# Performance work log

Hardware: AMD Instinct MI355X
Metric: run time of the kernel (lower is better)

## Reference

```python
import jax, jax.numpy as jnp
import numpy as np

B, T, H, LD = 32, 2048, 1024, 1024

def setup_inputs() -> dict:
    key = jax.random.key(0)
    k1, k2, k3, k4, k5 = jax.random.split(key, 5)
    scale = 1.0 / np.sqrt(H)
    return {
        "encoder_hidden": jax.random.normal(k1, (B, T, H), dtype=jnp.float32),
        "decoder_hidden": jax.random.normal(k2, (B, H), dtype=jnp.float32),
        "W1": jax.random.normal(k3, (H, LD), dtype=jnp.float32) * scale,
        "b1": jnp.zeros((LD,), dtype=jnp.float32),
        "W2": jax.random.normal(k4, (H, LD), dtype=jnp.float32) * scale,
        "b2": jnp.zeros((LD,), dtype=jnp.float32),
        "V": jax.random.normal(k5, (LD, 1), dtype=jnp.float32) * (1.0 / np.sqrt(LD)),
        "bV": jnp.zeros((1,), dtype=jnp.float32),
    }

def reference(encoder_hidden, decoder_hidden, W1, b1, W2, b2, V, bV):
    # dec proj: [B, 1, ld]
    dec_w = (decoder_hidden @ W1 + b1)[:, None, :]
    # enc proj: [B, T, ld]
    enc_w = jnp.einsum('bth,hl->btl', encoder_hidden, W2) + b2
    # multiplicative combine (as in source: decoder_Weight * encoder_weight)
    score = jnp.tanh(dec_w * enc_w) @ V + bV          # [B, T, 1]
    attn = jax.nn.softmax(score, axis=1)              # softmax over time
    context = jnp.sum(attn * encoder_hidden, axis=1)  # [B, H]
    return context, attn
```

## Files before the change

kernel.cpp:

```cpp
#include <hip/hip_runtime.h>
#include <hip/hip_bf16.h>
#include <math.h>

#define B_  32
#define T_  2048
#define H_  1024
#define LD_ 1024
#define M_  (B_*T_)

typedef __attribute__((ext_vector_type(8))) short bf16x8;
typedef __attribute__((ext_vector_type(4))) float f32x4;

__device__ __forceinline__ void async_copy16(void* lds, const void* g) {
  __builtin_amdgcn_global_load_lds(
      (const __attribute__((address_space(1))) void*)g,
      (__attribute__((address_space(3))) void*)lds, 16, 0, 0);
}

__global__ void convert_w2(const float* __restrict__ W2, __hip_bfloat16* __restrict__ w2p) {
  int idx = blockIdx.x * 256 + threadIdx.x;
  int kg = idx >> 10, n = idx & 1023;
  __align__(16) __hip_bfloat16 h[8];
#pragma unroll
  for (int j = 0; j < 8; ++j)
    h[j] = __float2bfloat16(W2[(size_t)(kg * 8 + j) * LD_ + n]);
  *reinterpret_cast<uint4*>(&w2p[(size_t)kg * (LD_ * 8) + n * 8]) =
      *reinterpret_cast<const uint4*>(h);
}

__global__ void dec_proj(const float* __restrict__ dec, const float* __restrict__ W1,
                         const float* __restrict__ b1, float* __restrict__ dec_w) {
  __shared__ float sdec[H_];
  int bb = blockIdx.x >> 2;
  int l = (blockIdx.x & 3) * 256 + threadIdx.x;
  for (int i = threadIdx.x; i < H_; i += 256) sdec[i] = dec[bb * H_ + i];
  __syncthreads();
  float a0 = 0.f, a1 = 0.f, a2 = 0.f, a3 = 0.f;
  for (int h = 0; h < H_; h += 4) {
    a0 += sdec[h + 0] * W1[(h + 0) * LD_ + l];
    a1 += sdec[h + 1] * W1[(h + 1) * LD_ + l];
    a2 += sdec[h + 2] * W1[(h + 2) * LD_ + l];
    a3 += sdec[h + 3] * W1[(h + 3) * LD_ + l];
  }
  dec_w[bb * LD_ + l] = (a0 + a1) + (a2 + a3) + b1[l];
}

__global__ __launch_bounds__(256, 2)
void score_gemm(const float* __restrict__ enc,
                const __hip_bfloat16* __restrict__ w2p,
                const float* __restrict__ dec_w,
                const float* __restrict__ b2,
                const float* __restrict__ V,
                float* __restrict__ score) {
  __shared__ __align__(16) __hip_bfloat16 Asm[4][128][8];
  __shared__ __align__(16) __hip_bfloat16 Bsm[4][256][8];

  const int tid  = threadIdx.x;
  const int lane = tid & 63;
  const int wave = tid >> 6;
  const int wm = wave >> 1, wn = wave & 1;
  const int nb = blockIdx.x, mb = blockIdx.y;
  const int row0 = mb * 128, col0 = nb * 256;
  const int q = lane >> 4, c15 = lane & 15;

  f32x4 acc[4][8] = {};

  const int sm  = tid >> 2;
  const int skg = tid & 3;

  for (int k0 = 0; k0 < H_; k0 += 32) {
#pragma unroll
    for (int pass = 0; pass < 2; ++pass) {
      int m = pass * 64 + sm;
      const float4* src = reinterpret_cast<const float4*>(
          enc + (size_t)(row0 + m) * H_ + k0 + skg * 8);
      float4 f0 = src[0], f1 = src[1];
      __align__(16) __hip_bfloat16 h[8];
      h[0] = __float2bfloat16(f0.x); h[1] = __float2bfloat16(f0.y);
      h[2] = __float2bfloat16(f0.z); h[3] = __float2bfloat16(f0.w);
      h[4] = __float2bfloat16(f1.x); h[5] = __float2bfloat16(f1.y);
      h[6] = __float2bfloat16(f1.z); h[7] = __float2bfloat16(f1.w);
      *reinterpret_cast<uint4*>(&Asm[skg][m][0]) = *reinterpret_cast<const uint4*>(h);
    }
    {
      char* bbase = (char*)&Bsm[0][0][0];
      const char* gbase = (const char*)w2p + ((size_t)(k0 >> 3)) * (LD_ * 8 * 2)
                          + (size_t)col0 * 16 + tid * 16;
#pragma unroll
      for (int p = 0; p < 4; ++p)
        async_copy16(bbase + p * 4096 + tid * 16, gbase + (size_t)p * (LD_ * 8 * 2));
    }
    __syncthreads();

    bf16x8 af[4], bfr[8];
#pragma unroll
    for (int i = 0; i < 4; ++i)
      af[i] = *reinterpret_cast<const bf16x8*>(&Asm[q][wm * 64 + i * 16 + c15][0]);
#pragma unroll
    for (int j = 0; j < 8; ++j)
      bfr[j] = *reinterpret_cast<const bf16x8*>(&Bsm[q][wn * 128 + j * 16 + c15][0]);
#pragma unroll
    for (int i = 0; i < 4; ++i)
#pragma unroll
      for (int j = 0; j < 8; ++j)
        acc[i][j] = __builtin_amdgcn_mfma_f32_16x16x32_bf16(af[i], bfr[j], acc[i][j], 0, 0, 0);
    __syncthreads();
  }

  const int bb = row0 >> 11;
  float b2v[8], dwv[8], Vv[8];
#pragma unroll
  for (int j = 0; j < 8; ++j) {
    int n = col0 + wn * 128 + j * 16 + c15;
    b2v[j] = b2[n];
    dwv[j] = dec_w[bb * LD_ + n];
    Vv[j]  = V[n];
  }
#pragma unroll
  for (int i = 0; i < 4; ++i) {
#pragma unroll
    for (int r = 0; r < 4; ++r) {
      float v = 0.f;
#pragma unroll
      for (int j = 0; j < 8; ++j) {
        float e = acc[i][j][r] + b2v[j];
        v += tanhf(dwv[j] * e) * Vv[j];
      }
      v += __shfl_xor(v, 1);
      v += __shfl_xor(v, 2);
      v += __shfl_xor(v, 4);
      v += __shfl_xor(v, 8);
      if (c15 == 0) {
        int row = row0 + wm * 64 + i * 16 + q * 4 + r;
        atomicAdd(&score[row], v);
      }
    }
  }
}

__global__ void softmax_k(const float* __restrict__ score, float* __restrict__ attn) {
  int bb = blockIdx.x;
  int tid = threadIdx.x;
  int lane = tid & 63, wave = tid >> 6;
  __shared__ float red[4];
  float v[8];
  float mx = -3.4e38f;
#pragma unroll
  for (int i = 0; i < 8; ++i) {
    v[i] = score[bb * T_ + i * 256 + tid];
    mx = fmaxf(mx, v[i]);
  }
#pragma unroll
  for (int m = 32; m >= 1; m >>= 1) mx = fmaxf(mx, __shfl_xor(mx, m));
  if (lane == 0) red[wave] = mx;
  __syncthreads();
  mx = fmaxf(fmaxf(red[0], red[1]), fmaxf(red[2], red[3]));
  __syncthreads();
  float s = 0.f;
#pragma unroll
  for (int i = 0; i < 8; ++i) { v[i] = __expf(v[i] - mx); s += v[i]; }
#pragma unroll
  for (int m = 32; m >= 1; m >>= 1) s += __shfl_xor(s, m);
  if (lane == 0) red[wave] = s;
  __syncthreads();
  s = red[0] + red[1] + red[2] + red[3];
  float inv = 1.f / s;
#pragma unroll
  for (int i = 0; i < 8; ++i) attn[bb * T_ + i * 256 + tid] = v[i] * inv;
}

__global__ void context_k(const float* __restrict__ enc, const float* __restrict__ attn,
                          float* __restrict__ ctx) {
  int bb = blockIdx.y;
  int hc = blockIdx.x & 3, tc = blockIdx.x >> 2;
  int h = hc * 256 + threadIdx.x;
  __shared__ float sat[512];
  int t0 = tc * 512;
  for (int i = threadIdx.x; i < 512; i += 256) sat[i] = attn[bb * T_ + t0 + i];
  __syncthreads();
  const float* base = enc + ((size_t)bb * T_ + t0) * H_ + h;
  float a0 = 0.f, a1 = 0.f, a2 = 0.f, a3 = 0.f;
  for (int t = 0; t < 512; t += 4) {
    a0 += sat[t + 0] * base[(size_t)(t + 0) * H_];
    a1 += sat[t + 1] * base[(size_t)(t + 1) * H_];
    a2 += sat[t + 2] * base[(size_t)(t + 2) * H_];
    a3 += sat[t + 3] * base[(size_t)(t + 3) * H_];
  }
  atomicAdd(&ctx[bb * H_ + h], (a0 + a1) + (a2 + a3));
}

extern "C" void kernel_launch(void* const* d_in, const int* in_sizes, int n_in,
                              void* d_out, int out_size, void* d_ws, size_t ws_size,
                              hipStream_t stream) {
  const float* enc = (const float*)d_in[0];
  const float* dec = (const float*)d_in[1];
  const float* W1  = (const float*)d_in[2];
  const float* b1  = (const float*)d_in[3];
  const float* W2  = (const float*)d_in[4];
  const float* b2  = (const float*)d_in[5];
  const float* V   = (const float*)d_in[6];

  char* ws = (char*)d_ws;
  __hip_bfloat16* w2p = (__hip_bfloat16*)ws;
  float* dec_w = (float*)(ws + (2u << 20));
  float* score = (float*)(ws + (2u << 20) + (128u << 10));

  float* out  = (float*)d_out;
  float* ctx  = out;
  float* attn = out + B_ * H_;

  hipMemsetAsync(score, 0, (size_t)M_ * sizeof(float), stream);
  hipMemsetAsync(ctx, 0, (size_t)B_ * H_ * sizeof(float), stream);

  convert_w2<<<(H_ * LD_ / 8) / 256, 256, 0, stream>>>(W2, w2p);
  dec_proj<<<B_ * 4, 256, 0, stream>>>(dec, W1, b1, dec_w);
  score_gemm<<<dim3(LD_ / 256, M_ / 128), 256, 0, stream>>>(enc, w2p, dec_w, b2, V, score);
  softmax_k<<<B_, 256, 0, stream>>>(score, attn);
  context_k<<<dim3(16, B_), 256, 0, stream>>>(enc, attn, ctx);
}
```

Measured before the change: 641.0 us.

## Double-buffer score GEMM tiles, swizzle LDS and block order, vectorize context

The score GEMM now double-buffers its LDS tiles. The next fp32 encoder tile is prefetched into registers and the next W2 tile is fetched asynchronously while MFMAs run on the current buffer, leaving one barrier per k-step. The A tile's LDS row index is XOR-swizzled to cut bank conflicts, and the block index is remapped so that co-resident blocks share encoder rows in cache. The context kernel is rewritten to read float4 per thread over 128 time steps with wider accumulators, which costs more LDS and registers in the GEMM and may lower occupancy.

```diff
diff --git a/kernel.cpp b/kernel.cpp
--- a/kernel.cpp
+++ b/kernel.cpp
@@ -52,14 +52,16 @@
                 const float* __restrict__ b2,
                 const float* __restrict__ V,
                 float* __restrict__ score) {
-  __shared__ __align__(16) __hip_bfloat16 Asm[4][128][8];
-  __shared__ __align__(16) __hip_bfloat16 Bsm[4][256][8];
+  __shared__ __align__(16) __hip_bfloat16 Asm[2][4][128][8];
+  __shared__ __align__(16) __hip_bfloat16 Bsm[2][4][256][8];
 
   const int tid  = threadIdx.x;
   const int lane = tid & 63;
   const int wave = tid >> 6;
   const int wm = wave >> 1, wn = wave & 1;
-  const int nb = blockIdx.x, mb = blockIdx.y;
+  const int bid = blockIdx.y * gridDim.x + blockIdx.x;
+  const int swz = (bid & 7) * 256 + (bid >> 3);
+  const int mb = swz >> 2, nb = swz & 3;
   const int row0 = mb * 128, col0 = nb * 256;
   const int q = lane >> 4, c15 = lane & 15;
 
@@ -67,43 +69,69 @@
 
   const int sm  = tid >> 2;
   const int skg = tid & 3;
-
-  for (int k0 = 0; k0 < H_; k0 += 32) {
-#pragma unroll
-    for (int pass = 0; pass < 2; ++pass) {
-      int m = pass * 64 + sm;
-      const float4* src = reinterpret_cast<const float4*>(
-          enc + (size_t)(row0 + m) * H_ + k0 + skg * 8);
-      float4 f0 = src[0], f1 = src[1];
-      __align__(16) __hip_bfloat16 h[8];
-      h[0] = __float2bfloat16(f0.x); h[1] = __float2bfloat16(f0.y);
-      h[2] = __float2bfloat16(f0.z); h[3] = __float2bfloat16(f0.w);
-      h[4] = __float2bfloat16(f1.x); h[5] = __float2bfloat16(f1.y);
-      h[6] = __float2bfloat16(f1.z); h[7] = __float2bfloat16(f1.w);
-      *reinterpret_cast<uint4*>(&Asm[skg][m][0]) = *reinterpret_cast<const uint4*>(h);
+  const int sx  = skg * 2;
+
+  const size_t arow0 = (size_t)(row0 + sm) * H_ + skg * 8;
+  const size_t arow1 = (size_t)(row0 + 64 + sm) * H_ + skg * 8;
+
+  float4 pf[4];
+
+  auto LOADA = [&](int k0) {
+    pf[0] = *reinterpret_cast<const float4*>(enc + arow0 + k0);
+    pf[1] = *reinterpret_cast<const float4*>(enc + arow0 + k0 + 4);
+    pf[2] = *reinterpret_cast<const float4*>(enc + arow1 + k0);
+    pf[3] = *reinterpret_cast<const float4*>(enc + arow1 + k0 + 4);
+  };
+  auto CVTW = [&](int buf) {
+    __align__(16) __hip_bfloat16 h[8];
+    h[0] = __float2bfloat16(pf[0].x); h[1] = __float2bfloat16(pf[0].y);
+    h[2] = __float2bfloat16(pf[0].z); h[3] = __float2bfloat16(pf[0].w);
+    h[4] = __float2bfloat16(pf[1].x); h[5] = __float2bfloat16(pf[1].y);
+    h[6] = __float2bfloat16(pf[1].z); h[7] = __float2bfloat16(pf[1].w);
+    *reinterpret_cast<uint4*>(&Asm[buf][skg][sm ^ sx][0]) =
+        *reinterpret_cast<const uint4*>(h);
+    h[0] = __float2bfloat16(pf[2].x); h[1] = __float2bfloat16(pf[2].y);
+    h[2] = __float2bfloat16(pf[2].z); h[3] = __float2bfloat16(pf[2].w);
+    h[4] = __float2bfloat16(pf[3].x); h[5] = __float2bfloat16(pf[3].y);
+    h[6] = __float2bfloat16(pf[3].z); h[7] = __float2bfloat16(pf[3].w);
+    *reinterpret_cast<uint4*>(&Asm[buf][skg][(64 + sm) ^ sx][0]) =
+        *reinterpret_cast<const uint4*>(h);
+  };
+  auto GLOADB = [&](int buf, int k0) {
+    char* bbase = (char*)&Bsm[buf][0][0][0] + tid * 16;
+    const char* gbase = (const char*)w2p + ((size_t)(k0 >> 3)) * (LD_ * 8 * 2)
+                        + (size_t)col0 * 16 + tid * 16;
+#pragma unroll
+    for (int p = 0; p < 4; ++p)
+      async_copy16(bbase + p * 4096, gbase + (size_t)p * (LD_ * 8 * 2));
+  };
+
+  LOADA(0);
+  GLOADB(0, 0);
+  CVTW(0);
+  __syncthreads();
+
+  for (int t = 0; t < 32; ++t) {
+    const int cur = t & 1;
+    if (t < 31) {
+      LOADA((t + 1) * 32);
+      GLOADB(cur ^ 1, (t + 1) * 32);
     }
-    {
-      char* bbase = (char*)&Bsm[0][0][0];
-      const char* gbase = (const char*)w2p + ((size_t)(k0 >> 3)) * (LD_ * 8 * 2)
-                          + (size_t)col0 * 16 + tid * 16;
-#pragma unroll
-      for (int p = 0; p < 4; ++p)
-        async_copy16(bbase + p * 4096 + tid * 16, gbase + (size_t)p * (LD_ * 8 * 2));
-    }
-    __syncthreads();
-
     bf16x8 af[4], bfr[8];
 #pragma unroll
     for (int i = 0; i < 4; ++i)
-      af[i] = *reinterpret_cast<const bf16x8*>(&Asm[q][wm * 64 + i * 16 + c15][0]);
+      af[i] = *reinterpret_cast<const bf16x8*>(
+          &Asm[cur][q][(wm * 64 + i * 16 + c15) ^ (q * 2)][0]);
 #pragma unroll
     for (int j = 0; j < 8; ++j)
-      bfr[j] = *reinterpret_cast<const bf16x8*>(&Bsm[q][wn * 128 + j * 16 + c15][0]);
+      bfr[j] = *reinterpret_cast<const bf16x8*>(
+          &Bsm[cur][q][wn * 128 + j * 16 + c15][0]);
 #pragma unroll
     for (int i = 0; i < 4; ++i)
 #pragma unroll
       for (int j = 0; j < 8; ++j)
         acc[i][j] = __builtin_amdgcn_mfma_f32_16x16x32_bf16(af[i], bfr[j], acc[i][j], 0, 0, 0);
+    if (t < 31) CVTW(cur ^ 1);
     __syncthreads();
   }
 
@@ -169,24 +197,34 @@
   for (int i = 0; i < 8; ++i) attn[bb * T_ + i * 256 + tid] = v[i] * inv;
 }
 
-__global__ void context_k(const float* __restrict__ enc, const float* __restrict__ attn,
-                          float* __restrict__ ctx) {
-  int bb = blockIdx.y;
-  int hc = blockIdx.x & 3, tc = blockIdx.x >> 2;
-  int h = hc * 256 + threadIdx.x;
-  __shared__ float sat[512];
-  int t0 = tc * 512;
-  for (int i = threadIdx.x; i < 512; i += 256) sat[i] = attn[bb * T_ + t0 + i];
-  __syncthreads();
-  const float* base = enc + ((size_t)bb * T_ + t0) * H_ + h;
-  float a0 = 0.f, a1 = 0.f, a2 = 0.f, a3 = 0.f;
-  for (int t = 0; t < 512; t += 4) {
-    a0 += sat[t + 0] * base[(size_t)(t + 0) * H_];
-    a1 += sat[t + 1] * base[(size_t)(t + 1) * H_];
-    a2 += sat[t + 2] * base[(size_t)(t + 2) * H_];
-    a3 += sat[t + 3] * base[(size_t)(t + 3) * H_];
-  }
-  atomicAdd(&ctx[bb * H_ + h], (a0 + a1) + (a2 + a3));
+__global__ __launch_bounds__(256)
+void context_k(const float* __restrict__ enc, const float* __restrict__ attn,
+               float* __restrict__ ctx) {
+  const int bb = blockIdx.y;
+  const int t0 = blockIdx.x * 128;
+  __shared__ float sat[128];
+  if (threadIdx.x < 128) sat[threadIdx.x] = attn[bb * T_ + t0 + threadIdx.x];
+  __syncthreads();
+  const float4* base = reinterpret_cast<const float4*>(
+      enc + ((size_t)bb * T_ + t0) * H_) + threadIdx.x;
+  f32x4 a0 = {}, a1 = {}, a2 = {}, a3 = {};
+  for (int t = 0; t < 128; t += 8) {
+    float4 v[8];
+#pragma unroll
+    for (int u = 0; u < 8; ++u) v[u] = base[(size_t)(t + u) * (H_ / 4)];
+#pragma unroll
+    for (int u = 0; u < 8; ++u) {
+      float a = sat[t + u];
+      f32x4& d = (u & 2) ? ((u & 1) ? a3 : a2) : ((u & 1) ? a1 : a0);
+      d[0] += a * v[u].x; d[1] += a * v[u].y;
+      d[2] += a * v[u].z; d[3] += a * v[u].w;
+    }
+  }
+  const int h = threadIdx.x * 4;
+  atomicAdd(&ctx[bb * H_ + h + 0], (a0[0] + a1[0]) + (a2[0] + a3[0]));
+  atomicAdd(&ctx[bb * H_ + h + 1], (a0[1] + a1[1]) + (a2[1] + a3[1]));
+  atomicAdd(&ctx[bb * H_ + h + 2], (a0[2] + a1[2]) + (a2[2] + a3[2]));
+  atomicAdd(&ctx[bb * H_ + h + 3], (a0[3] + a1[3]) + (a2[3] + a3[3]));
 }
 
 extern "C" void kernel_launch(void* const* d_in, const int* in_sizes, int n_in,
```

New measurement: 699.3 us. +9.1%, slower.
